# Optimization experiments

Measured on AMD Instinct MI355X. Metric: run time of the kernel, lower is better.

Reference implementation:

```python
import jax, jax.numpy as jnp
import numpy as np

B, S, D, H = 2, 2048, 1024, 16
DK = D // H


def setup_inputs() -> dict:
    key = jax.random.key(0)
    ks = jax.random.split(key, 8)
    w_scale = 1.0 / np.sqrt(D)
    return {
        "query": jax.random.normal(ks[0], (B, S, D), jnp.float32),
        "key": jax.random.normal(ks[1], (B, S, D), jnp.float32),
        "value": jax.random.normal(ks[2], (B, S, D), jnp.float32),
        "Wq": jax.random.normal(ks[3], (D, D), jnp.float32) * w_scale,
        "bq": jnp.zeros((D,), jnp.float32),
        "Wk": jax.random.normal(ks[4], (D, D), jnp.float32) * w_scale,
        "bk": jnp.zeros((D,), jnp.float32),
        "Wv": jax.random.normal(ks[5], (D, D), jnp.float32) * w_scale,
        "bv": jnp.zeros((D,), jnp.float32),
        "Wo": jax.random.normal(ks[6], (D, D), jnp.float32) * w_scale,
        "bo": jnp.zeros((D,), jnp.float32),
    }


def _heads(x, W, b):
    # torch nn.Linear: y = x @ W.T + b ; then [B,S,D] -> [B,H,S,DK]
    y = x @ W.T + b
    return y.reshape(x.shape[0], x.shape[1], H, DK).transpose(0, 2, 1, 3)


def reference(query, key, value, Wq, bq, Wk, bk, Wv, bv, Wo, bo):
    q = _heads(query, Wq, bq)   # [B,H,S,DK]
    k = _heads(key, Wk, bk)
    v = _heads(value, Wv, bv)
    scale = 100.0 / np.sqrt(DK).astype(np.float32)
    scores = jnp.einsum("bhqd,bhkd->bhqk", q, k) * scale  # [B,H,Sq,Sk]
    prob = jax.nn.softmax(scores, axis=-1)                 # dropout p=0 -> identity
    out = jnp.einsum("bhqk,bhkd->bhqd", prob, v)           # [B,H,Sq,DK]
    mean_atp = prob.mean(axis=(1, 2))                      # mean over heads & query -> [B,Sk]
    out = out.transpose(0, 2, 1, 3).reshape(query.shape[0], -1, D)
    out = out @ Wo.T + bo
    return out, mean_atp
```

## Files before the change

kernel.cpp:

```cpp
#include <hip/hip_runtime.h>
#include <hip/hip_bf16.h>


#define B_  2
#define S_  2048
#define D_  1024
#define H_  16
#define DK_ 64

typedef __bf16 bf16x8 __attribute__((ext_vector_type(8)));
typedef float f32x4  __attribute__((ext_vector_type(4)));

__device__ __forceinline__ void ld_g2l16(const __bf16* g, __bf16* l) {
  __builtin_amdgcn_global_load_lds(
      (const __attribute__((address_space(1))) void*)g,
      (__attribute__((address_space(3))) void*)l, 16, 0, 0);
}

__global__ __launch_bounds__(256)
void split3_kernel(const float* __restrict__ x, __bf16* __restrict__ y,
                   int n, int mode)
{
  int i = (blockIdx.x * 256 + threadIdx.x) * 8;
  if (i >= n) return;
  float4 a = *(const float4*)(x + i);
  float4 b = *(const float4*)(x + i + 4);
  float xs[8] = {a.x, a.y, a.z, a.w, b.x, b.y, b.z, b.w};
  __bf16 out[24];
#pragma unroll
  for (int j = 0; j < 8; j++) {
    float v = xs[j];
    __bf16 hi = (__bf16)v;
    __bf16 lo = (__bf16)(v - (float)hi);
    if (mode == 0) { out[3*j] = hi; out[3*j+1] = hi; out[3*j+2] = lo; }
    else           { out[3*j] = hi; out[3*j+1] = lo; out[3*j+2] = hi; }
  }
  *(bf16x8*)(y + 3 * (size_t)i)      = *(bf16x8*)&out[0];
  *(bf16x8*)(y + 3 * (size_t)i + 8)  = *(bf16x8*)&out[8];
  *(bf16x8*)(y + 3 * (size_t)i + 16) = *(bf16x8*)&out[16];
}

__global__ __launch_bounds__(256)
void tobf16_kernel(const float* __restrict__ x, __bf16* __restrict__ y, int n)
{
  int i = (blockIdx.x * 256 + threadIdx.x) * 8;
  if (i >= n) return;
  float4 a = *(const float4*)(x + i);
  float4 b = *(const float4*)(x + i + 4);
  __bf16 out[8] = {(__bf16)a.x, (__bf16)a.y, (__bf16)a.z, (__bf16)a.w,
                   (__bf16)b.x, (__bf16)b.y, (__bf16)b.z, (__bf16)b.w};
  *(bf16x8*)(y + i) = *(bf16x8*)&out[0];
}

#define TM 128
#define TN 128
#define TK 64

__global__ __launch_bounds__(256)
void gemm_mfma(const __bf16* __restrict__ X, const __bf16* __restrict__ W,
               const float* __restrict__ bias, void* __restrict__ Y,
               void* __restrict__ Y2, int M, int N, int K, int out_mode)
{
  __shared__ __align__(16) __bf16 Xa[TM * TK];
  __shared__ __align__(16) __bf16 Wb[TN * TK];

  const int tid  = threadIdx.x;
  const int lane = tid & 63;
  const int w    = tid >> 6;
  const int c    = lane & 15;
  const int quad = lane >> 4;
  const int row0 = blockIdx.y * TM;
  const int col0 = blockIdx.x * TN;
  const int wr   = (w >> 1) * 64;
  const int wc   = (w & 1) * 64;

  f32x4 acc[4][4];
#pragma unroll
  for (int i = 0; i < 4; i++)
#pragma unroll
    for (int j = 0; j < 4; j++) acc[i][j] = (f32x4){0.f, 0.f, 0.f, 0.f};

  for (int k0 = 0; k0 < K; k0 += TK) {
    __syncthreads();
#pragma unroll
    for (int i = 0; i < 4; i++) {
      int chunk = w * 256 + i * 64 + lane;
      int r = chunk >> 3, dch = chunk & 7;
      ld_g2l16(X + (size_t)(row0 + r) * K + k0 + dch * 8, &Xa[chunk * 8]);
      ld_g2l16(W + (size_t)(col0 + r) * K + k0 + dch * 8, &Wb[chunk * 8]);
    }
    __syncthreads();

#pragma unroll
    for (int cc = 0; cc < 2; cc++) {
      bf16x8 af[4], bf[4];
#pragma unroll
      for (int i = 0; i < 4; i++)
        af[i] = *(const bf16x8*)&Xa[(wr + i * 16 + c) * TK + cc * 32 + quad * 8];
#pragma unroll
      for (int j = 0; j < 4; j++)
        bf[j] = *(const bf16x8*)&Wb[(wc + j * 16 + c) * TK + cc * 32 + quad * 8];
#pragma unroll
      for (int i = 0; i < 4; i++)
#pragma unroll
        for (int j = 0; j < 4; j++)
          acc[i][j] = __builtin_amdgcn_mfma_f32_16x16x32_bf16(af[i], bf[j],
                                                              acc[i][j], 0, 0, 0);
    }
  }

#pragma unroll
  for (int i = 0; i < 4; i++) {
#pragma unroll
    for (int j = 0; j < 4; j++) {
      int col = col0 + wc + j * 16 + c;
      float bcol = bias[col];
#pragma unroll
      for (int r = 0; r < 4; r++) {
        int row = row0 + wr + i * 16 + quad * 4 + r;
        float v = acc[i][j][r] + bcol;
        if (out_mode == 0) {
          ((float*)Y)[(size_t)row * N + col] = v;
        } else {
          int b2 = row >> 11, s = row & (S_ - 1);
          int h = col >> 6, dk = col & 63;
          if (out_mode == 1) {
            size_t off = ((size_t)(b2 * H_ + h) * S_ + s) * DK_ + dk;
            __bf16 hi = (__bf16)v;
            ((__bf16*)Y)[off]  = hi;
            ((__bf16*)Y2)[off] = (__bf16)(v - (float)hi);
          } else {
            ((__bf16*)Y)[((size_t)(b2 * H_ + h) * DK_ + dk) * S_ + s] = (__bf16)v;
          }
        }
      }
    }
  }
}

#define LSTR 72
#define PSTR 68

__device__ __forceinline__ void qk_scores(const __bf16* __restrict__ Kh,
                                          const __bf16* __restrict__ Kl,
                                          const bf16x8 qhf[2][2],
                                          const bf16x8 qlf[2][2],
                                          int c, int quad, f32x4 sc[2][4])
{
#pragma unroll
  for (int nt = 0; nt < 4; nt++) {
#pragma unroll
    for (int rg = 0; rg < 2; rg++) sc[rg][nt] = (f32x4){0.f, 0.f, 0.f, 0.f};
#pragma unroll
    for (int cc = 0; cc < 2; cc++) {
      bf16x8 bh8 = *(const bf16x8*)&Kh[(nt * 16 + c) * LSTR + cc * 32 + quad * 8];
      bf16x8 bl8 = *(const bf16x8*)&Kl[(nt * 16 + c) * LSTR + cc * 32 + quad * 8];
#pragma unroll
      for (int rg = 0; rg < 2; rg++) {
        sc[rg][nt] = __builtin_amdgcn_mfma_f32_16x16x32_bf16(qhf[rg][cc], bh8,
                                                             sc[rg][nt], 0, 0, 0);
        sc[rg][nt] = __builtin_amdgcn_mfma_f32_16x16x32_bf16(qhf[rg][cc], bl8,
                                                             sc[rg][nt], 0, 0, 0);
        sc[rg][nt] = __builtin_amdgcn_mfma_f32_16x16x32_bf16(qlf[rg][cc], bh8,
                                                             sc[rg][nt], 0, 0, 0);
      }
    }
  }
}

__global__ __launch_bounds__(256)
void attn_mfma(const __bf16* __restrict__ qh_ws, const __bf16* __restrict__ ql_ws,
               const __bf16* __restrict__ kh_ws, const __bf16* __restrict__ kl_ws,
               const __bf16* __restrict__ vt_ws, __bf16* __restrict__ attn_out,
               float* __restrict__ atp_out)
{
  __shared__ __align__(16) __bf16 Kh[64 * LSTR];
  __shared__ __align__(16) __bf16 Kl[64 * LSTR];
  __shared__ __align__(16) __bf16 Vt[64 * LSTR];
  __shared__ __align__(16) float  Ps[4][32 * PSTR];
  __shared__ float  atp_lds[S_];

  const int tid  = threadIdx.x;
  const int lane = tid & 63;
  const int w    = tid >> 6;
  const int c    = lane & 15;
  const int quad = lane >> 4;
  const int qb   = blockIdx.x;
  const int h    = blockIdx.y;
  const int b    = blockIdx.z;

  const size_t bh = (size_t)(b * H_ + h);
  const __bf16* qhg = qh_ws + (bh * S_ + qb * 128) * DK_;
  const __bf16* qlg = ql_ws + (bh * S_ + qb * 128) * DK_;
  const __bf16* khg = kh_ws + bh * S_ * DK_;
  const __bf16* klg = kl_ws + bh * S_ * DK_;
  const __bf16* vg  = vt_ws + bh * DK_ * S_;

  bf16x8 qhf[2][2], qlf[2][2];
#pragma unroll
  for (int rg = 0; rg < 2; rg++) {
    const __bf16* qrow = qhg + (size_t)(w * 32 + rg * 16 + c) * DK_;
    qhf[rg][0] = *(const bf16x8*)(qrow + quad * 8);
    qhf[rg][1] = *(const bf16x8*)(qrow + 32 + quad * 8);
    const __bf16* qrow2 = qlg + (size_t)(w * 32 + rg * 16 + c) * DK_;
    qlf[rg][0] = *(const bf16x8*)(qrow2 + quad * 8);
    qlf[rg][1] = *(const bf16x8*)(qrow2 + 32 + quad * 8);
  }

  const float scale = 12.5f;
  float m_r[2][4], l_r[2][4];
#pragma unroll
  for (int rg = 0; rg < 2; rg++)
#pragma unroll
    for (int r = 0; r < 4; r++) { m_r[rg][r] = -1e30f; l_r[rg][r] = 0.f; }

  for (int kt = 0; kt < S_ / 64; kt++) {
    __syncthreads();
#pragma unroll
    for (int i = 0; i < 2; i++) {
      int idx = i * 256 + tid;
      int key = idx >> 3, dch = idx & 7;
      *(bf16x8*)&Kh[key * LSTR + dch * 8] =
          *(const bf16x8*)(khg + (size_t)(kt * 64 + key) * DK_ + dch * 8);
      *(bf16x8*)&Kl[key * LSTR + dch * 8] =
          *(const bf16x8*)(klg + (size_t)(kt * 64 + key) * DK_ + dch * 8);
    }
    __syncthreads();

    f32x4 sc[2][4];
    qk_scores(Kh, Kl, qhf, qlf, c, quad, sc);

    float tm[2][4], psum[2][4];
#pragma unroll
    for (int rg = 0; rg < 2; rg++)
#pragma unroll
      for (int r = 0; r < 4; r++) {
        tm[rg][r] = fmaxf(fmaxf(sc[rg][0][r], sc[rg][1][r]),
                          fmaxf(sc[rg][2][r], sc[rg][3][r])) * scale;
      }
#pragma unroll
    for (int o = 1; o < 16; o <<= 1)
#pragma unroll
      for (int rg = 0; rg < 2; rg++)
#pragma unroll
        for (int r = 0; r < 4; r++)
          tm[rg][r] = fmaxf(tm[rg][r], __shfl_xor(tm[rg][r], o, 64));

#pragma unroll
    for (int rg = 0; rg < 2; rg++)
#pragma unroll
      for (int r = 0; r < 4; r++) {
        float mnew = fmaxf(m_r[rg][r], tm[rg][r]);
        float p = 0.f;
#pragma unroll
        for (int nt = 0; nt < 4; nt++) p += __expf(sc[rg][nt][r] * scale - mnew);
        psum[rg][r] = p;
        l_r[rg][r] *= __expf(m_r[rg][r] - mnew);
        m_r[rg][r] = mnew;
      }
#pragma unroll
    for (int o = 1; o < 16; o <<= 1)
#pragma unroll
      for (int rg = 0; rg < 2; rg++)
#pragma unroll
        for (int r = 0; r < 4; r++)
          psum[rg][r] += __shfl_xor(psum[rg][r], o, 64);
#pragma unroll
    for (int rg = 0; rg < 2; rg++)
#pragma unroll
      for (int r = 0; r < 4; r++) l_r[rg][r] += psum[rg][r];
  }

  float rl[2][4];
#pragma unroll
  for (int rg = 0; rg < 2; rg++)
#pragma unroll
    for (int r = 0; r < 4; r++) rl[rg][r] = 1.0f / l_r[rg][r];

  for (int i = tid; i < S_; i += 256) atp_lds[i] = 0.f;

  f32x4 of[2][4];
#pragma unroll
  for (int rg = 0; rg < 2; rg++)
#pragma unroll
    for (int nt = 0; nt < 4; nt++) of[rg][nt] = (f32x4){0.f, 0.f, 0.f, 0.f};

  float* ps = Ps[w];

  for (int kt = 0; kt < S_ / 64; kt++) {
    __syncthreads();
#pragma unroll
    for (int i = 0; i < 2; i++) {
      int idx = i * 256 + tid;
      int key = idx >> 3, dch = idx & 7;
      *(bf16x8*)&Kh[key * LSTR + dch * 8] =
          *(const bf16x8*)(khg + (size_t)(kt * 64 + key) * DK_ + dch * 8);
      *(bf16x8*)&Kl[key * LSTR + dch * 8] =
          *(const bf16x8*)(klg + (size_t)(kt * 64 + key) * DK_ + dch * 8);
      *(bf16x8*)&Vt[key * LSTR + dch * 8] =
          *(const bf16x8*)(vg + (size_t)key * S_ + kt * 64 + dch * 8);
    }
    __syncthreads();

    f32x4 sc[2][4];
    qk_scores(Kh, Kl, qhf, qlf, c, quad, sc);

#pragma unroll
    for (int nt = 0; nt < 4; nt++) {
      float t = 0.f;
#pragma unroll
      for (int rg = 0; rg < 2; rg++)
#pragma unroll
        for (int r = 0; r < 4; r++) {
          float p = __expf(sc[rg][nt][r] * scale - m_r[rg][r]) * rl[rg][r];
          ps[(rg * 16 + quad * 4 + r) * PSTR + nt * 16 + c] = p;
          t += p;
        }
      t += __shfl_xor(t, 16, 64);
      t += __shfl_xor(t, 32, 64);
      if (quad == 0) atomicAdd(&atp_lds[kt * 64 + nt * 16 + c], t);
    }

#pragma unroll
    for (int rg = 0; rg < 2; rg++) {
      bf16x8 pa[2];
#pragma unroll
      for (int cc = 0; cc < 2; cc++) {
        const float* pp = &ps[(rg * 16 + c) * PSTR + cc * 32 + quad * 8];
        f32x4 p0 = *(const f32x4*)pp;
        f32x4 p1 = *(const f32x4*)(pp + 4);
        bf16x8 v8;
#pragma unroll
        for (int j = 0; j < 4; j++) { v8[j] = (__bf16)p0[j]; v8[4 + j] = (__bf16)p1[j]; }
        pa[cc] = v8;
      }
#pragma unroll
      for (int nt = 0; nt < 4; nt++)
#pragma unroll
        for (int cc = 0; cc < 2; cc++) {
          bf16x8 vb = *(const bf16x8*)&Vt[(nt * 16 + c) * LSTR + cc * 32 + quad * 8];
          of[rg][nt] = __builtin_amdgcn_mfma_f32_16x16x32_bf16(pa[cc], vb,
                                                               of[rg][nt], 0, 0, 0);
        }
    }
  }

#pragma unroll
  for (int rg = 0; rg < 2; rg++)
#pragma unroll
    for (int nt = 0; nt < 4; nt++)
#pragma unroll
      for (int r = 0; r < 4; r++)
        attn_out[((size_t)(b * S_ + qb * 128 + w * 32 + rg * 16 + quad * 4 + r)) * D_
                 + h * DK_ + nt * 16 + c] = (__bf16)of[rg][nt][r];

  __syncthreads();
  const float inv = 1.0f / ((float)H_ * (float)S_);
  for (int i = tid; i < S_; i += 256)
    atomicAdd(&atp_out[b * S_ + i], atp_lds[i] * inv);
}

__global__ void zero_f32(float* __restrict__ p, int n) {
  int i = blockIdx.x * 256 + threadIdx.x;
  if (i < n) p[i] = 0.f;
}

extern "C" void kernel_launch(void* const* d_in, const int* in_sizes, int n_in,
                              void* d_out, int out_size, void* d_ws, size_t ws_size,
                              hipStream_t stream)
{
  const float* query = (const float*)d_in[0];
  const float* key_  = (const float*)d_in[1];
  const float* value = (const float*)d_in[2];
  const float* Wq = (const float*)d_in[3];
  const float* bq = (const float*)d_in[4];
  const float* Wk = (const float*)d_in[5];
  const float* bk = (const float*)d_in[6];
  const float* Wv = (const float*)d_in[7];
  const float* bv = (const float*)d_in[8];
  const float* Wo = (const float*)d_in[9];
  const float* bo = (const float*)d_in[10];

  float* out = (float*)d_out;
  float* atp = out + (size_t)B_ * S_ * D_;

  const size_t NE = (size_t)B_ * S_ * D_;
  const size_t NW = (size_t)D_ * D_;
  __bf16* p = (__bf16*)d_ws;
  __bf16* qcat3 = p;               p += 3 * NE;
  __bf16* kcat3 = p;               p += 3 * NE;
  __bf16* wqc3  = p;               p += 3 * NW;
  __bf16* wkc3  = p;               p += 3 * NW;
  __bf16* vxb   = p;               p += NE;
  __bf16* wvb   = p;               p += NW;
  __bf16* wob   = p;               p += NW;
  __bf16* qh_ws = p;               p += NE;
  __bf16* ql_ws = p;               p += NE;
  __bf16* kh_ws = p;               p += NE;
  __bf16* kl_ws = p;               p += NE;
  __bf16* vt_ws = kcat3;
  __bf16* a_ws  = qcat3;

  const int M = B_ * S_;

  split3_kernel<<<NE / (256 * 8), 256, 0, stream>>>(query, qcat3, (int)NE, 0);
  split3_kernel<<<NE / (256 * 8), 256, 0, stream>>>(key_,  kcat3, (int)NE, 0);
  split3_kernel<<<NW / (256 * 8), 256, 0, stream>>>(Wq, wqc3, (int)NW, 1);
  split3_kernel<<<NW / (256 * 8), 256, 0, stream>>>(Wk, wkc3, (int)NW, 1);
  tobf16_kernel<<<NE / (256 * 8), 256, 0, stream>>>(value, vxb, (int)NE);
  tobf16_kernel<<<NW / (256 * 8), 256, 0, stream>>>(Wv, wvb, (int)NW);
  tobf16_kernel<<<NW / (256 * 8), 256, 0, stream>>>(Wo, wob, (int)NW);

  dim3 ggrid(D_ / TN, M / TM);
  gemm_mfma<<<ggrid, 256, 0, stream>>>(qcat3, wqc3, bq, qh_ws, ql_ws, M, D_, 3 * D_, 1);
  gemm_mfma<<<ggrid, 256, 0, stream>>>(kcat3, wkc3, bk, kh_ws, kl_ws, M, D_, 3 * D_, 1);
  gemm_mfma<<<ggrid, 256, 0, stream>>>(vxb,   wvb,  bv, vt_ws, nullptr, M, D_, D_, 2);

  zero_f32<<<(B_ * S_ + 255) / 256, 256, 0, stream>>>(atp, B_ * S_);

  attn_mfma<<<dim3(S_ / 128, H_, B_), 256, 0, stream>>>(qh_ws, ql_ws, kh_ws, kl_ws,
                                                        vt_ws, a_ws, atp);

  gemm_mfma<<<ggrid, 256, 0, stream>>>(a_ws, wob, bo, out, nullptr, M, D_, D_, 0);
}
```

Measured before the change: 543.4 us.

## Fuse conversions, fold softmax scale into Q, halve GEMM M-tile, shrink P buffer

Merges the seven fp32-to-bf16 conversion launches into one kernel that dispatches on block index. Folds scale*log2(e) into the Q projection epilogue so the attention softmax can use exp2f without per-element multiplies. Halves the GEMM M tile to 64, which doubles the block count for better CU occupancy but lowers per-block reuse. Also interleaves the P write and PV MFMA per row group so the P LDS buffer can shrink and the atp reductions are deferred. Pre-scaling Q before the hi/lo split changes rounding slightly.

```diff
diff --git a/kernel.cpp b/kernel.cpp
--- a/kernel.cpp
+++ b/kernel.cpp
@@ -17,12 +17,11 @@
       (__attribute__((address_space(3))) void*)l, 16, 0, 0);
 }
 
-__global__ __launch_bounds__(256)
-void split3_kernel(const float* __restrict__ x, __bf16* __restrict__ y,
-                   int n, int mode)
-{
-  int i = (blockIdx.x * 256 + threadIdx.x) * 8;
-  if (i >= n) return;
+__device__ __forceinline__ void split3_body(const float* __restrict__ x,
+                                            __bf16* __restrict__ y,
+                                            int lbid, int tid, int mode)
+{
+  int i = (lbid * 256 + tid) * 8;
   float4 a = *(const float4*)(x + i);
   float4 b = *(const float4*)(x + i + 4);
   float xs[8] = {a.x, a.y, a.z, a.w, b.x, b.y, b.z, b.w};
@@ -40,11 +39,11 @@
   *(bf16x8*)(y + 3 * (size_t)i + 16) = *(bf16x8*)&out[16];
 }
 
-__global__ __launch_bounds__(256)
-void tobf16_kernel(const float* __restrict__ x, __bf16* __restrict__ y, int n)
-{
-  int i = (blockIdx.x * 256 + threadIdx.x) * 8;
-  if (i >= n) return;
+__device__ __forceinline__ void tobf16_body(const float* __restrict__ x,
+                                            __bf16* __restrict__ y,
+                                            int lbid, int tid)
+{
+  int i = (lbid * 256 + tid) * 8;
   float4 a = *(const float4*)(x + i);
   float4 b = *(const float4*)(x + i + 4);
   __bf16 out[8] = {(__bf16)a.x, (__bf16)a.y, (__bf16)a.z, (__bf16)a.w,
@@ -52,14 +51,34 @@
   *(bf16x8*)(y + i) = *(bf16x8*)&out[0];
 }
 
-#define TM 128
+__global__ __launch_bounds__(256)
+void convert_all(const float* __restrict__ query, const float* __restrict__ key_,
+                 const float* __restrict__ value, const float* __restrict__ Wq,
+                 const float* __restrict__ Wk, const float* __restrict__ Wv,
+                 const float* __restrict__ Wo, __bf16* __restrict__ qcat3,
+                 __bf16* __restrict__ kcat3, __bf16* __restrict__ vxb,
+                 __bf16* __restrict__ wqc3, __bf16* __restrict__ wkc3,
+                 __bf16* __restrict__ wvb, __bf16* __restrict__ wob)
+{
+  int bid = blockIdx.x, tid = threadIdx.x;
+  if (bid < 2048)       split3_body(query, qcat3, bid, tid, 0);
+  else if (bid < 4096)  split3_body(key_,  kcat3, bid - 2048, tid, 0);
+  else if (bid < 6144)  tobf16_body(value, vxb,   bid - 4096, tid);
+  else if (bid < 6656)  split3_body(Wq, wqc3, bid - 6144, tid, 1);
+  else if (bid < 7168)  split3_body(Wk, wkc3, bid - 6656, tid, 1);
+  else if (bid < 7680)  tobf16_body(Wv, wvb, bid - 7168, tid);
+  else                  tobf16_body(Wo, wob, bid - 7680, tid);
+}
+
+#define TM 64
 #define TN 128
 #define TK 64
 
 __global__ __launch_bounds__(256)
 void gemm_mfma(const __bf16* __restrict__ X, const __bf16* __restrict__ W,
                const float* __restrict__ bias, void* __restrict__ Y,
-               void* __restrict__ Y2, int M, int N, int K, int out_mode)
+               void* __restrict__ Y2, int M, int N, int K, int out_mode,
+               float osf)
 {
   __shared__ __align__(16) __bf16 Xa[TM * TK];
   __shared__ __align__(16) __bf16 Wb[TN * TK];
@@ -71,39 +90,43 @@
   const int quad = lane >> 4;
   const int row0 = blockIdx.y * TM;
   const int col0 = blockIdx.x * TN;
-  const int wr   = (w >> 1) * 64;
-  const int wc   = (w & 1) * 64;
-
-  f32x4 acc[4][4];
+  const int wc   = w * 32;
+
+  f32x4 acc[4][2];
 #pragma unroll
   for (int i = 0; i < 4; i++)
 #pragma unroll
-    for (int j = 0; j < 4; j++) acc[i][j] = (f32x4){0.f, 0.f, 0.f, 0.f};
+    for (int j = 0; j < 2; j++) acc[i][j] = (f32x4){0.f, 0.f, 0.f, 0.f};
 
   for (int k0 = 0; k0 < K; k0 += TK) {
     __syncthreads();
 #pragma unroll
-    for (int i = 0; i < 4; i++) {
-      int chunk = w * 256 + i * 64 + lane;
+    for (int i = 0; i < 2; i++) {
+      int chunk = i * 256 + w * 64 + lane;
       int r = chunk >> 3, dch = chunk & 7;
       ld_g2l16(X + (size_t)(row0 + r) * K + k0 + dch * 8, &Xa[chunk * 8]);
+    }
+#pragma unroll
+    for (int i = 0; i < 4; i++) {
+      int chunk = i * 256 + w * 64 + lane;
+      int r = chunk >> 3, dch = chunk & 7;
       ld_g2l16(W + (size_t)(col0 + r) * K + k0 + dch * 8, &Wb[chunk * 8]);
     }
     __syncthreads();
 
 #pragma unroll
     for (int cc = 0; cc < 2; cc++) {
-      bf16x8 af[4], bf[4];
+      bf16x8 af[4], bf[2];
 #pragma unroll
       for (int i = 0; i < 4; i++)
-        af[i] = *(const bf16x8*)&Xa[(wr + i * 16 + c) * TK + cc * 32 + quad * 8];
-#pragma unroll
-      for (int j = 0; j < 4; j++)
+        af[i] = *(const bf16x8*)&Xa[(i * 16 + c) * TK + cc * 32 + quad * 8];
+#pragma unroll
+      for (int j = 0; j < 2; j++)
         bf[j] = *(const bf16x8*)&Wb[(wc + j * 16 + c) * TK + cc * 32 + quad * 8];
 #pragma unroll
       for (int i = 0; i < 4; i++)
 #pragma unroll
-        for (int j = 0; j < 4; j++)
+        for (int j = 0; j < 2; j++)
           acc[i][j] = __builtin_amdgcn_mfma_f32_16x16x32_bf16(af[i], bf[j],
                                                               acc[i][j], 0, 0, 0);
     }
@@ -112,13 +135,13 @@
 #pragma unroll
   for (int i = 0; i < 4; i++) {
 #pragma unroll
-    for (int j = 0; j < 4; j++) {
+    for (int j = 0; j < 2; j++) {
       int col = col0 + wc + j * 16 + c;
       float bcol = bias[col];
 #pragma unroll
       for (int r = 0; r < 4; r++) {
-        int row = row0 + wr + i * 16 + quad * 4 + r;
-        float v = acc[i][j][r] + bcol;
+        int row = row0 + i * 16 + quad * 4 + r;
+        float v = (acc[i][j][r] + bcol) * osf;
         if (out_mode == 0) {
           ((float*)Y)[(size_t)row * N + col] = v;
         } else {
@@ -177,7 +200,7 @@
   __shared__ __align__(16) __bf16 Kh[64 * LSTR];
   __shared__ __align__(16) __bf16 Kl[64 * LSTR];
   __shared__ __align__(16) __bf16 Vt[64 * LSTR];
-  __shared__ __align__(16) float  Ps[4][32 * PSTR];
+  __shared__ __align__(16) float  Ps[4][16 * PSTR];
   __shared__ float  atp_lds[S_];
 
   const int tid  = threadIdx.x;
@@ -207,7 +230,6 @@
     qlf[rg][1] = *(const bf16x8*)(qrow2 + 32 + quad * 8);
   }
 
-  const float scale = 12.5f;
   float m_r[2][4], l_r[2][4];
 #pragma unroll
   for (int rg = 0; rg < 2; rg++)
@@ -234,10 +256,9 @@
 #pragma unroll
     for (int rg = 0; rg < 2; rg++)
 #pragma unroll
-      for (int r = 0; r < 4; r++) {
+      for (int r = 0; r < 4; r++)
         tm[rg][r] = fmaxf(fmaxf(sc[rg][0][r], sc[rg][1][r]),
-                          fmaxf(sc[rg][2][r], sc[rg][3][r])) * scale;
-      }
+                          fmaxf(sc[rg][2][r], sc[rg][3][r]));
 #pragma unroll
     for (int o = 1; o < 16; o <<= 1)
 #pragma unroll
@@ -253,9 +274,9 @@
         float mnew = fmaxf(m_r[rg][r], tm[rg][r]);
         float p = 0.f;
 #pragma unroll
-        for (int nt = 0; nt < 4; nt++) p += __expf(sc[rg][nt][r] * scale - mnew);
+        for (int nt = 0; nt < 4; nt++) p += exp2f(sc[rg][nt][r] - mnew);
         psum[rg][r] = p;
-        l_r[rg][r] *= __expf(m_r[rg][r] - mnew);
+        l_r[rg][r] *= exp2f(m_r[rg][r] - mnew);
         m_r[rg][r] = mnew;
       }
 #pragma unroll
@@ -305,28 +326,21 @@
     f32x4 sc[2][4];
     qk_scores(Kh, Kl, qhf, qlf, c, quad, sc);
 
-#pragma unroll
-    for (int nt = 0; nt < 4; nt++) {
-      float t = 0.f;
-#pragma unroll
-      for (int rg = 0; rg < 2; rg++)
+    float t[4] = {0.f, 0.f, 0.f, 0.f};
+#pragma unroll
+    for (int rg = 0; rg < 2; rg++) {
+#pragma unroll
+      for (int nt = 0; nt < 4; nt++)
 #pragma unroll
         for (int r = 0; r < 4; r++) {
-          float p = __expf(sc[rg][nt][r] * scale - m_r[rg][r]) * rl[rg][r];
-          ps[(rg * 16 + quad * 4 + r) * PSTR + nt * 16 + c] = p;
-          t += p;
+          float p = exp2f(sc[rg][nt][r] - m_r[rg][r]) * rl[rg][r];
+          ps[(quad * 4 + r) * PSTR + nt * 16 + c] = p;
+          t[nt] += p;
         }
-      t += __shfl_xor(t, 16, 64);
-      t += __shfl_xor(t, 32, 64);
-      if (quad == 0) atomicAdd(&atp_lds[kt * 64 + nt * 16 + c], t);
-    }
-
-#pragma unroll
-    for (int rg = 0; rg < 2; rg++) {
       bf16x8 pa[2];
 #pragma unroll
       for (int cc = 0; cc < 2; cc++) {
-        const float* pp = &ps[(rg * 16 + c) * PSTR + cc * 32 + quad * 8];
+        const float* pp = &ps[c * PSTR + cc * 32 + quad * 8];
         f32x4 p0 = *(const f32x4*)pp;
         f32x4 p1 = *(const f32x4*)(pp + 4);
         bf16x8 v8;
@@ -342,6 +356,14 @@
           of[rg][nt] = __builtin_amdgcn_mfma_f32_16x16x32_bf16(pa[cc], vb,
                                                                of[rg][nt], 0, 0, 0);
         }
+    }
+
+#pragma unroll
+    for (int nt = 0; nt < 4; nt++) {
+      float tt = t[nt];
+      tt += __shfl_xor(tt, 16, 64);
+      tt += __shfl_xor(tt, 32, 64);
+      if (quad == 0) atomicAdd(&atp_lds[kt * 64 + nt * 16 + c], tt);
     }
   }
 
@@ -402,24 +424,20 @@
   __bf16* a_ws  = qcat3;
 
   const int M = B_ * S_;
-
-  split3_kernel<<<NE / (256 * 8), 256, 0, stream>>>(query, qcat3, (int)NE, 0);
-  split3_kernel<<<NE / (256 * 8), 256, 0, stream>>>(key_,  kcat3, (int)NE, 0);
-  split3_kernel<<<NW / (256 * 8), 256, 0, stream>>>(Wq, wqc3, (int)NW, 1);
-  split3_kernel<<<NW / (256 * 8), 256, 0, stream>>>(Wk, wkc3, (int)NW, 1);
-  tobf16_kernel<<<NE / (256 * 8), 256, 0, stream>>>(value, vxb, (int)NE);
-  tobf16_kernel<<<NW / (256 * 8), 256, 0, stream>>>(Wv, wvb, (int)NW);
-  tobf16_kernel<<<NW / (256 * 8), 256, 0, stream>>>(Wo, wob, (int)NW);
+  const float QSF = 18.0337320f;
+
+  convert_all<<<8192, 256, 0, stream>>>(query, key_, value, Wq, Wk, Wv, Wo,
+                                        qcat3, kcat3, vxb, wqc3, wkc3, wvb, wob);
 
   dim3 ggrid(D_ / TN, M / TM);
-  gemm_mfma<<<ggrid, 256, 0, stream>>>(qcat3, wqc3, bq, qh_ws, ql_ws, M, D_, 3 * D_, 1);
-  gemm_mfma<<<ggrid, 256, 0, stream>>>(kcat3, wkc3, bk, kh_ws, kl_ws, M, D_, 3 * D_, 1);
-  gemm_mfma<<<ggrid, 256, 0, stream>>>(vxb,   wvb,  bv, vt_ws, nullptr, M, D_, D_, 2);
+  gemm_mfma<<<ggrid, 256, 0, stream>>>(qcat3, wqc3, bq, qh_ws, ql_ws, M, D_, 3 * D_, 1, QSF);
+  gemm_mfma<<<ggrid, 256, 0, stream>>>(kcat3, wkc3, bk, kh_ws, kl_ws, M, D_, 3 * D_, 1, 1.0f);
+  gemm_mfma<<<ggrid, 256, 0, stream>>>(vxb,   wvb,  bv, vt_ws, nullptr, M, D_, D_, 2, 1.0f);
 
   zero_f32<<<(B_ * S_ + 255) / 256, 256, 0, stream>>>(atp, B_ * S_);
 
   attn_mfma<<<dim3(S_ / 128, H_, B_), 256, 0, stream>>>(qh_ws, ql_ws, kh_ws, kl_ws,
                                                         vt_ws, a_ws, atp);
 
-  gemm_mfma<<<ggrid, 256, 0, stream>>>(a_ws, wob, bo, out, nullptr, M, D_, D_, 0);
-}
+  gemm_mfma<<<ggrid, 256, 0, stream>>>(a_ws, wob, bo, out, nullptr, M, D_, D_, 0, 1.0f);
+}
```

Measured after the change: 511.3 us. -5.9%, faster.
